# Optimization experiments

Measured on AMD Instinct MI355X. Metric: run time of the kernel, lower is better.

Reference implementation:

```python
import jax, jax.numpy as jnp
import numpy as np

EPS = 1e-6
NORM_FACTOR = 1000.0  # self.normalization_factor, aggregation 'sum'

# ---- Lorentz manifold (curvature -1, hyperboloid <x,x>_L = -1) ----

def _linner(x, y):
    # Lorentz inner product, keepdim on last axis
    return -x[..., :1] * y[..., :1] + jnp.sum(x[..., 1:] * y[..., 1:], axis=-1, keepdims=True)

def _proj_tan0(u):
    return jnp.concatenate([jnp.zeros_like(u[..., :1]), u[..., 1:]], axis=-1)

def _expmap0(u):
    sp = u[..., 1:]
    n = jnp.sqrt(jnp.clip(jnp.sum(sp * sp, axis=-1, keepdims=True), EPS))
    return jnp.concatenate([jnp.cosh(n), jnp.sinh(n) / n * sp], axis=-1)

def _logmap0(x):
    x0 = jnp.clip(x[..., :1], 1.0 + EPS)
    d = jnp.arccosh(x0)
    sp = x[..., 1:] * (d / jnp.sqrt(x0 * x0 - 1.0))
    return jnp.concatenate([jnp.zeros_like(x0), sp], axis=-1)

def _dist(x, y):
    return jnp.arccosh(jnp.clip(-_linner(x, y), 1.0 + EPS))

def _logmap(x, y):
    alpha = jnp.clip(-_linner(x, y), 1.0 + EPS)
    u = y - alpha * x                      # y + <x,y>_L x
    return jnp.arccosh(alpha) * u / jnp.sqrt(alpha * alpha - 1.0)

def _expmap(x, u):
    n = jnp.sqrt(jnp.clip(_linner(u, u), EPS))
    return jnp.cosh(n) * x + jnp.sinh(n) / n * u

def _proju(x, u):
    return u + _linner(x, u) * x

def _transp0(y, v):
    # parallel transport from origin o=(1,0,...,0) to y
    coef = _linner(y, v) / (1.0 + y[..., :1])
    oy = jnp.concatenate([y[..., :1] + 1.0, y[..., 1:]], axis=-1)
    return v + coef * oy

def _layernorm(x, g, b, eps=1e-5):
    m = jnp.mean(x, axis=-1, keepdims=True)
    v = jnp.mean((x - m) ** 2, axis=-1, keepdims=True)
    return (x - m) / jnp.sqrt(v + eps) * g + b


def setup_inputs() -> dict:
    N, E, D, ED = 10000, 320000, 128, 2
    key = jax.random.key(0)
    ks = jax.random.split(key, 10)
    # nodes on the hyperboloid: expmap0 of a small tangent vector
    h_tan = 0.02 * jax.random.normal(ks[0], (N, D), dtype=jnp.float32)
    h = _expmap0(_proj_tan0(h_tan))
    edge_attr = jax.random.normal(ks[1], (E, ED), dtype=jnp.float32)
    row = jax.random.randint(ks[2], (E,), 0, N, dtype=jnp.int32)
    col = jax.random.randint(ks[3], (E,), 0, N, dtype=jnp.int32)
    node_mask = jnp.ones((N, 1), dtype=jnp.float32)
    edge_mask = jnp.ones((E, 1), dtype=jnp.float32)
    s = 1.0 / np.sqrt(D)
    W = s * jax.random.normal(ks[4], (D, D), dtype=jnp.float32)
    bias = 0.0 * jax.random.normal(ks[5], (1, D), dtype=jnp.float32)  # init.constant_(bias, 0)
    att_in = 2 * D + ED + 1  # x_row, x_col, edge_attr + geodesic
    att_w1 = (1.0 / np.sqrt(att_in)) * jax.random.normal(ks[6], (att_in, D), dtype=jnp.float32)
    att_b1 = jnp.zeros((D,), dtype=jnp.float32)
    att_w2 = s * jax.random.normal(ks[7], (D, 1), dtype=jnp.float32)
    att_b2 = jnp.zeros((1,), dtype=jnp.float32)
    ln_gamma = jnp.ones((D - 1,), dtype=jnp.float32)
    ln_beta = jnp.zeros((D - 1,), dtype=jnp.float32)
    return {"h": h, "edge_attr": edge_attr, "row": row, "col": col,
            "node_mask": node_mask, "edge_mask": edge_mask, "W": W, "bias": bias,
            "att_w1": att_w1, "att_b1": att_b1, "att_w2": att_w2, "att_b2": att_b2,
            "ln_gamma": ln_gamma, "ln_beta": ln_beta}


def reference(h, edge_attr, row, col, node_mask, edge_mask, W, bias,
              att_w1, att_b1, att_w2, att_b2, ln_gamma, ln_beta):
    N = h.shape[0]
    # ---- HypLinear ----
    xt = _logmap0(h) @ W                  # Linear(in,out,bias=False)
    x = _expmap0(_proj_tan0(xt))
    b = _transp0(x, _proj_tan0(bias))
    x = _expmap(x, b)
    # ---- HypAgg ----
    x_tan = _logmap0(x)
    xr, xc = x[row], x[col]
    geo = _dist(xr, xc)                   # [E,1]
    att_in = jnp.concatenate([x_tan[row], x_tan[col], edge_attr, geo], axis=-1)
    hid = jax.nn.silu(att_in @ att_w1 + att_b1)
    att = jax.nn.sigmoid(hid @ att_w2 + att_b2) * edge_mask   # [E,1]
    loc = _logmap(xr, xc)                 # [E,D]
    agg = jax.ops.segment_sum(loc * att, row, num_segments=N) / NORM_FACTOR
    x = _expmap(x, _proju(x, agg))
    # ---- HNorm (Lorentz: LN on spatial components only) ----
    ht = _logmap0(x)
    sp = _layernorm(ht[..., 1:], ln_gamma, ln_beta)
    x = _expmap0(jnp.concatenate([ht[..., :1], sp], axis=-1))
    # ---- HypAct (manifold_out = Lorentz as well) ----
    xt = _proj_tan0(jax.nn.silu(_logmap0(x)))
    return _expmap0(xt)
```

## Files before the change

kernel.cpp:

```cpp
#include <hip/hip_runtime.h>
#include <math.h>

#define D 128
#define NPB 8
#define EPS1 (1.0f + 1e-6f)

__device__ __forceinline__ float sum16(float v) {
#pragma unroll
    for (int o = 8; o; o >>= 1) v += __shfl_xor(v, o, 64);
    return v;
}

__device__ __forceinline__ float facosh(float a) {
    return __logf(a + sqrtf(fmaxf(a * a - 1.0f, 0.0f)));
}

__device__ __forceinline__ void unpack8(const float4& a, const float4& b,
                                        float* d) {
    d[0] = a.x; d[1] = a.y; d[2] = a.z; d[3] = a.w;
    d[4] = b.x; d[5] = b.y; d[6] = b.z; d[7] = b.w;
}

__device__ __forceinline__ void bsumH(float* v, float (*wred)[4], int lane,
                                      int wid, int kp) {
    __syncthreads();
#pragma unroll
    for (int o = 32; o; o >>= 1)
#pragma unroll
        for (int nl = 0; nl < 4; nl++) v[nl] += __shfl_xor(v[nl], o, 64);
    if (lane == 0)
#pragma unroll
        for (int nl = 0; nl < 4; nl++) wred[wid][nl] = v[nl];
    __syncthreads();
#pragma unroll
    for (int nl = 0; nl < 4; nl++)
        v[nl] = wred[2 * kp][nl] + wred[2 * kp + 1][nl];
}

__global__ __launch_bounds__(256) void node_pre8(
    const float* __restrict__ h, const float* __restrict__ W,
    const float* __restrict__ bias, const float* __restrict__ att_w1,
    const float* __restrict__ att_b1, float* __restrict__ XQ,
    float* __restrict__ P_out, const int* __restrict__ row,
    int* __restrict__ cnt, int N, int E) {
    int i0 = blockIdx.x * NPB;
    int tid = threadIdx.x;
    int j = tid & 127, kp = tid >> 7;
    int lane = tid & 63, wid = tid >> 6;
    int nbase = kp * 4;
    __shared__ __align__(16) float t8[NPB][D];
    __shared__ float psumP[2][NPB][D];
    __shared__ float psumQ[2][NPB][D];
    __shared__ float wred[4][4];

    float hj[4];
#pragma unroll
    for (int nl = 0; nl < 4; nl++) {
        int gi = i0 + nbase + nl;
        hj[nl] = (gi < N) ? h[(size_t)gi * D + j] : 0.0f;
        t8[nbase + nl][j] = hj[nl];
    }
    __syncthreads();
    float tj[4];
#pragma unroll
    for (int nl = 0; nl < 4; nl++) {
        float h0 = fmaxf(t8[nbase + nl][0], EPS1);
        float fac = facosh(h0) * rsqrtf(h0 * h0 - 1.0f);
        tj[nl] = (j == 0) ? 0.0f : hj[nl] * fac;
    }
    __syncthreads();
#pragma unroll
    for (int nl = 0; nl < 4; nl++) t8[nbase + nl][j] = tj[nl];
    __syncthreads();

    float xtp[NPB];
#pragma unroll
    for (int n = 0; n < NPB; n++) xtp[n] = 0.0f;
    int kbeg = kp * 64;
    for (int k0 = kbeg; k0 < kbeg + 64; k0 += 4) {
        float w0 = W[(k0 + 0) * D + j], w1 = W[(k0 + 1) * D + j];
        float w2 = W[(k0 + 2) * D + j], w3 = W[(k0 + 3) * D + j];
#pragma unroll
        for (int n = 0; n < NPB; n++) {
            float4 tv = *(const float4*)&t8[n][k0];
            xtp[n] = fmaf(tv.x, w0,
                          fmaf(tv.y, w1, fmaf(tv.z, w2, fmaf(tv.w, w3, xtp[n]))));
        }
    }
#pragma unroll
    for (int n = 0; n < NPB; n++) psumP[kp][n][j] = xtp[n];
    __syncthreads();
    float xt[4];
#pragma unroll
    for (int nl = 0; nl < 4; nl++) {
        int n = nbase + nl;
        xt[nl] = (j == 0) ? 0.0f : (psumP[0][n][j] + psumP[1][n][j]);
    }

    float v4[4];
#pragma unroll
    for (int nl = 0; nl < 4; nl++) v4[nl] = xt[nl] * xt[nl];
    bsumH(v4, wred, lane, wid, kp);
    float xj[4];
#pragma unroll
    for (int nl = 0; nl < 4; nl++) {
        float nn = sqrtf(fmaxf(v4[nl], 1e-6f));
        float e = __expf(nn), ei = __fdividef(1.0f, e);
        float ch = 0.5f * (e + ei), sh = 0.5f * (e - ei);
        xj[nl] = (j == 0) ? ch : __fdividef(sh, nn) * xt[nl];
    }

    float vj = (j == 0) ? 0.0f : bias[j];
#pragma unroll
    for (int nl = 0; nl < 4; nl++) v4[nl] = xj[nl] * vj;
    bsumH(v4, wred, lane, wid, kp);
    __syncthreads();
#pragma unroll
    for (int nl = 0; nl < 4; nl++) t8[nbase + nl][j] = xj[nl];
    __syncthreads();
    float bj[4];
#pragma unroll
    for (int nl = 0; nl < 4; nl++) {
        float X0 = t8[nbase + nl][0];
        float coef = __fdividef(v4[nl], 1.0f + X0);
        bj[nl] = vj + coef * ((j == 0) ? (X0 + 1.0f) : xj[nl]);
    }
#pragma unroll
    for (int nl = 0; nl < 4; nl++)
        v4[nl] = (j == 0) ? -bj[nl] * bj[nl] : bj[nl] * bj[nl];
    bsumH(v4, wred, lane, wid, kp);
    float xnj[4];
#pragma unroll
    for (int nl = 0; nl < 4; nl++) {
        float nb = sqrtf(fmaxf(v4[nl], 1e-6f));
        float e = __expf(nb), ei = __fdividef(1.0f, e);
        float ch = 0.5f * (e + ei), sh = 0.5f * (e - ei);
        xnj[nl] = ch * xj[nl] + __fdividef(sh, nb) * bj[nl];
        int gi = i0 + nbase + nl;
        if (gi < N) XQ[(size_t)gi * 256 + j] = xnj[nl];
    }

    __syncthreads();
#pragma unroll
    for (int nl = 0; nl < 4; nl++) t8[nbase + nl][j] = xnj[nl];
    __syncthreads();
    float xtj[4];
#pragma unroll
    for (int nl = 0; nl < 4; nl++) {
        float Y0 = fmaxf(t8[nbase + nl][0], EPS1);
        float f = facosh(Y0) * rsqrtf(Y0 * Y0 - 1.0f);
        xtj[nl] = (j == 0) ? 0.0f : xnj[nl] * f;
    }
    __syncthreads();
#pragma unroll
    for (int nl = 0; nl < 4; nl++) t8[nbase + nl][j] = xtj[nl];
    __syncthreads();

    float pp[NPB], qq[NPB];
#pragma unroll
    for (int n = 0; n < NPB; n++) {
        pp[n] = 0.0f;
        qq[n] = 0.0f;
    }
    for (int k0 = kbeg; k0 < kbeg + 64; k0 += 4) {
        float a0 = att_w1[(k0 + 0) * D + j], a1 = att_w1[(k0 + 1) * D + j];
        float a2 = att_w1[(k0 + 2) * D + j], a3 = att_w1[(k0 + 3) * D + j];
        float c0 = att_w1[(D + k0 + 0) * D + j], c1 = att_w1[(D + k0 + 1) * D + j];
        float c2 = att_w1[(D + k0 + 2) * D + j], c3 = att_w1[(D + k0 + 3) * D + j];
#pragma unroll
        for (int n = 0; n < NPB; n++) {
            float4 tv = *(const float4*)&t8[n][k0];
            pp[n] = fmaf(tv.x, a0,
                         fmaf(tv.y, a1, fmaf(tv.z, a2, fmaf(tv.w, a3, pp[n]))));
            qq[n] = fmaf(tv.x, c0,
                         fmaf(tv.y, c1, fmaf(tv.z, c2, fmaf(tv.w, c3, qq[n]))));
        }
    }
#pragma unroll
    for (int n = 0; n < NPB; n++) {
        psumP[kp][n][j] = pp[n];
        psumQ[kp][n][j] = qq[n];
    }
    __syncthreads();
    float b1 = att_b1[j];
#pragma unroll
    for (int nl = 0; nl < 4; nl++) {
        int n = nbase + nl;
        int gi = i0 + n;
        if (gi < N) {
            P_out[(size_t)gi * D + j] = psumP[0][n][j] + psumP[1][n][j] + b1;
            XQ[(size_t)gi * 256 + 128 + j] = psumQ[0][n][j] + psumQ[1][n][j];
        }
    }

    int gtid = blockIdx.x * 256 + tid;
    int tot = gridDim.x * 256;
    for (int e2 = gtid; e2 < E; e2 += tot) atomicAdd(&cnt[row[e2]], 1);
}

__global__ __launch_bounds__(1024) void scan_kernel(const int* __restrict__ cnt,
                                                    int* __restrict__ off,
                                                    int* __restrict__ cursor,
                                                    int N) {
    __shared__ int wsum[16];
    __shared__ int carry_s;
    int tid = threadIdx.x, lane = tid & 63, wid = tid >> 6;
    if (tid == 0) carry_s = 0;
    __syncthreads();
    for (int base = 0; base < N; base += 1024) {
        int idx = base + tid;
        int v = (idx < N) ? cnt[idx] : 0;
        int orig = v;
#pragma unroll
        for (int o = 1; o < 64; o <<= 1) {
            int t = __shfl_up(v, o, 64);
            if (lane >= o) v += t;
        }
        if (lane == 63) wsum[wid] = v;
        __syncthreads();
        if (wid == 0 && lane < 16) {
            int w = wsum[lane];
#pragma unroll
            for (int o = 1; o < 16; o <<= 1) {
                int t = __shfl_up(w, o, 64);
                if (lane >= o) w += t;
            }
            wsum[lane] = w;
        }
        __syncthreads();
        int carry = carry_s;
        int wbase = (wid == 0) ? 0 : wsum[wid - 1];
        int excl = carry + wbase + v - orig;
        if (idx < N) {
            off[idx] = excl;
            cursor[idx] = excl;
        }
        __syncthreads();
        if (tid == 1023) carry_s = carry + wsum[15];
        __syncthreads();
    }
}

__global__ void scatter_kernel(const int* __restrict__ row,
                               const int* __restrict__ col,
                               const float* __restrict__ edge_attr,
                               const float* __restrict__ edge_mask,
                               int* __restrict__ cursor,
                               float4* __restrict__ rec, int E) {
    const float2* ea2 = (const float2*)edge_attr;
    for (int e = blockIdx.x * blockDim.x + threadIdx.x; e < E;
         e += gridDim.x * blockDim.x) {
        int r = row[e];
        int pos = atomicAdd(&cursor[r], 1);
        float2 a = ea2[e];
        rec[pos] = make_float4(__int_as_float(col[e]), a.x, a.y, edge_mask[e]);
    }
}

__global__ __launch_bounds__(256) void edge_agg(
    const float* __restrict__ XQ, const float* __restrict__ P,
    const float4* __restrict__ rec, const int* __restrict__ off,
    const int* __restrict__ cnt, const float* __restrict__ w1c,
    const float* __restrict__ att_w2, const float* __restrict__ att_b2,
    float* __restrict__ agg, int N) {
    int tid = threadIdx.x, lane = tid & 63;
    int sub = lane & 15, grp = lane >> 4;
    int i = blockIdx.x * 4 + (tid >> 6);
    bool valid = i < N;
    i = min(i, N - 1);
    int f4 = sub * 2;

    const float4* w4 = (const float4*)w1c;
    const float4* aw4 = (const float4*)att_w2;
    const float4* xq4r = (const float4*)(XQ + (size_t)i * 256);
    const float4* pr4 = (const float4*)(P + (size_t)i * D);
    float xr[8], pr[8], wa[8], wb[8], wg[8], w2v[8];
    unpack8(xq4r[f4], xq4r[f4 + 1], xr);
    unpack8(pr4[f4], pr4[f4 + 1], pr);
    unpack8(w4[f4], w4[f4 + 1], wa);
    unpack8(w4[32 + f4], w4[32 + f4 + 1], wb);
    unpack8(w4[64 + f4], w4[64 + f4 + 1], wg);
    unpack8(aw4[f4], aw4[f4 + 1], w2v);
    float b2 = att_b2[0];
    float xr0s = (sub == 0) ? -xr[0] : xr[0];

    float acc[8];
#pragma unroll
    for (int u = 0; u < 8; u++) acc[u] = 0.0f;

    int s = off[i], m = valid ? cnt[i] : 0;
    int clen = (m + 3) >> 2;
    int k0 = grp * clen;
    int len = min(m, k0 + clen) - k0;

    auto compute2 = [&](const float4& rc1, const float4& a0, const float4& a1,
                        const float4& a2, const float4& a3, bool act1,
                        const float4& rc2, const float4& b0, const float4& b1,
                        const float4& b2q, const float4& b3, bool act2) {
        float xc1[8], qc1[8], xc2[8], qc2[8];
        unpack8(a0, a1, xc1);
        unpack8(a2, a3, qc1);
        unpack8(b0, b1, xc2);
        unpack8(b2q, b3, qc2);
        float lin1 = xr0s * xc1[0];
        float lin2 = xr0s * xc2[0];
#pragma unroll
        for (int u = 1; u < 8; u++) {
            lin1 = fmaf(xr[u], xc1[u], lin1);
            lin2 = fmaf(xr[u], xc2[u], lin2);
        }
#pragma unroll
        for (int o = 8; o; o >>= 1) {
            lin1 += __shfl_xor(lin1, o, 64);
            lin2 += __shfl_xor(lin2, o, 64);
        }
        float alpha1 = fmaxf(-lin1, EPS1);
        float alpha2 = fmaxf(-lin2, EPS1);
        float a2m1 = fmaxf(fmaf(alpha1, alpha1, -1.0f), 1e-12f);
        float a2m2 = fmaxf(fmaf(alpha2, alpha2, -1.0f), 1e-12f);
        float rden1 = rsqrtf(a2m1);
        float rden2 = rsqrtf(a2m2);
        float geo1 = __logf(fmaf(a2m1, rden1, alpha1));
        float geo2 = __logf(fmaf(a2m2, rden2, alpha2));
        float lp1 = 0.0f, lp2 = 0.0f;
#pragma unroll
        for (int u = 0; u < 8; u++) {
            float hv1 = pr[u] + qc1[u] +
                        fmaf(rc1.y, wa[u], fmaf(rc1.z, wb[u], geo1 * wg[u]));
            float hv2 = pr[u] + qc2[u] +
                        fmaf(rc2.y, wa[u], fmaf(rc2.z, wb[u], geo2 * wg[u]));
            float sg1 = __fdividef(1.0f, 1.0f + __expf(-hv1));
            float sg2 = __fdividef(1.0f, 1.0f + __expf(-hv2));
            lp1 = fmaf(hv1 * sg1, w2v[u], lp1);
            lp2 = fmaf(hv2 * sg2, w2v[u], lp2);
        }
#pragma unroll
        for (int o = 8; o; o >>= 1) {
            lp1 += __shfl_xor(lp1, o, 64);
            lp2 += __shfl_xor(lp2, o, 64);
        }
        float w1 = act1 ? rc1.w : 0.0f;
        float w2 = act2 ? rc2.w : 0.0f;
        float att1 = w1 * __fdividef(1.0f, 1.0f + __expf(-(lp1 + b2)));
        float att2 = w2 * __fdividef(1.0f, 1.0f + __expf(-(lp2 + b2)));
        float sc1 = att1 * geo1 * rden1 * 1e-3f;
        float sc2 = att2 * geo2 * rden2 * 1e-3f;
#pragma unroll
        for (int u = 0; u < 8; u++) {
            acc[u] = fmaf(sc1, fmaf(-alpha1, xr[u], xc1[u]), acc[u]);
            acc[u] = fmaf(sc2, fmaf(-alpha2, xr[u], xc2[u]), acc[u]);
        }
    };

    float4 z = make_float4(__int_as_float(0), 0.0f, 0.0f, 0.0f);
    float4 rcA = z, rcB = z, rcC, rcD;
    if (len > 0) rcA = rec[s + k0];
    if (len > 1) rcB = rec[s + k0 + 1];
    const float4* pA = (const float4*)(XQ + (size_t)__float_as_int(rcA.x) * 256);
    const float4* pB = (const float4*)(XQ + (size_t)__float_as_int(rcB.x) * 256);
    float4 gA0 = pA[f4], gA1 = pA[f4 + 1], gA2 = pA[32 + f4],
           gA3 = pA[32 + f4 + 1];
    float4 gB0 = pB[f4], gB1 = pB[f4 + 1], gB2 = pB[32 + f4],
           gB3 = pB[32 + f4 + 1];

    for (int t = 0; t < clen; t += 2) {
        rcC = rcA;
        if (t + 2 < len) rcC = rec[s + k0 + t + 2];
        rcD = rcB;
        if (t + 3 < len) rcD = rec[s + k0 + t + 3];
        const float4* pC =
            (const float4*)(XQ + (size_t)__float_as_int(rcC.x) * 256);
        const float4* pD =
            (const float4*)(XQ + (size_t)__float_as_int(rcD.x) * 256);
        float4 gC0 = pC[f4], gC1 = pC[f4 + 1], gC2 = pC[32 + f4],
               gC3 = pC[32 + f4 + 1];
        float4 gD0 = pD[f4], gD1 = pD[f4 + 1], gD2 = pD[32 + f4],
               gD3 = pD[32 + f4 + 1];
        compute2(rcA, gA0, gA1, gA2, gA3, t < len, rcB, gB0, gB1, gB2, gB3,
                 t + 1 < len);
        rcA = rcC; rcB = rcD;
        gA0 = gC0; gA1 = gC1; gA2 = gC2; gA3 = gC3;
        gB0 = gD0; gB1 = gD1; gB2 = gD2; gB3 = gD3;
    }

#pragma unroll
    for (int u = 0; u < 8; u++) {
        acc[u] += __shfl_xor(acc[u], 16, 64);
        acc[u] += __shfl_xor(acc[u], 32, 64);
    }
    if (valid && grp == 0) {
        float4* a4 = (float4*)(agg + (size_t)i * D);
        a4[f4] = make_float4(acc[0], acc[1], acc[2], acc[3]);
        a4[f4 + 1] = make_float4(acc[4], acc[5], acc[6], acc[7]);
    }
}

__global__ __launch_bounds__(256) void node_post(
    const float* __restrict__ XQ, const float* __restrict__ agg,
    const float* __restrict__ gamma, const float* __restrict__ beta,
    float* __restrict__ out, int N) {
    int tid = threadIdx.x, lane = tid & 63;
    int sub = lane & 15;
    int i = blockIdx.x * 16 + (tid >> 4);
    bool valid = i < N;
    i = min(i, N - 1);
    int j8 = sub * 8, f4 = sub * 2;

    const float4* xq4r = (const float4*)(XQ + (size_t)i * 256);
    const float4* ag4 = (const float4*)(agg + (size_t)i * D);
    float xr[8], acc[8];
    unpack8(xq4r[f4], xq4r[f4 + 1], xr);
    unpack8(ag4[f4], ag4[f4 + 1], acc);

    float lxa_p = (sub == 0) ? -xr[0] * acc[0] : xr[0] * acc[0];
#pragma unroll
    for (int u = 1; u < 8; u++) lxa_p = fmaf(xr[u], acc[u], lxa_p);
    float lxa = sum16(lxa_p);
    float uj[8];
#pragma unroll
    for (int u = 0; u < 8; u++) uj[u] = fmaf(lxa, xr[u], acc[u]);
    float luu_p = (sub == 0) ? -uj[0] * uj[0] : uj[0] * uj[0];
#pragma unroll
    for (int u = 1; u < 8; u++) luu_p = fmaf(uj[u], uj[u], luu_p);
    float luu = sum16(luu_p);
    float nn = sqrtf(fmaxf(luu, 1e-6f));
    float e = __expf(nn), ei = __fdividef(1.0f, e);
    float ch = 0.5f * (e + ei), shv = __fdividef(0.5f * (e - ei), nn);
    float xn[8];
#pragma unroll
    for (int u = 0; u < 8; u++) xn[u] = ch * xr[u] + shv * uj[u];
    float X0 = __shfl(xn[0], lane & 48, 64);
    X0 = fmaxf(X0, EPS1);
    float fc = facosh(X0) * rsqrtf(X0 * X0 - 1.0f);
    float ht[8];
#pragma unroll
    for (int u = 0; u < 8; u++) ht[u] = xn[u] * fc;
    if (sub == 0) ht[0] = 0.0f;
    float mp = 0.0f;
#pragma unroll
    for (int u = 0; u < 8; u++) mp += ht[u];
    float mean = sum16(mp) * (1.0f / 127.0f);
    float diff[8];
#pragma unroll
    for (int u = 0; u < 8; u++) diff[u] = ht[u] - mean;
    if (sub == 0) diff[0] = 0.0f;
    float vp = 0.0f;
#pragma unroll
    for (int u = 0; u < 8; u++) vp = fmaf(diff[u], diff[u], vp);
    float var = sum16(vp) * (1.0f / 127.0f);
    float rstd = rsqrtf(var + 1e-5f);
    float sp[8];
#pragma unroll
    for (int u = 0; u < 8; u++) {
        int j = j8 + u;
        sp[u] = (j > 0) ? fmaf(diff[u] * rstd, gamma[j - 1], beta[j - 1]) : 0.0f;
    }
    float n2p = 0.0f;
#pragma unroll
    for (int u = 0; u < 8; u++) n2p = fmaf(sp[u], sp[u], n2p);
    float n2 = sqrtf(fmaxf(sum16(n2p), 1e-6f));
    e = __expf(n2);
    ei = __fdividef(1.0f, e);
    float y0 = 0.5f * (e + ei), sh2 = __fdividef(0.5f * (e - ei), n2);
    float yj[8];
#pragma unroll
    for (int u = 0; u < 8; u++) yj[u] = sh2 * sp[u];
    if (sub == 0) yj[0] = y0;
    float y0c = fmaxf(y0, EPS1);
    float f3 = facosh(y0c) * rsqrtf(y0c * y0c - 1.0f);
    float sj[8];
#pragma unroll
    for (int u = 0; u < 8; u++) {
        float lj = yj[u] * f3;
        sj[u] = __fdividef(lj, 1.0f + __expf(-lj));
    }
    if (sub == 0) sj[0] = 0.0f;
    float n3p = 0.0f;
#pragma unroll
    for (int u = 0; u < 8; u++) n3p = fmaf(sj[u], sj[u], n3p);
    float n3 = sqrtf(fmaxf(sum16(n3p), 1e-6f));
    e = __expf(n3);
    ei = __fdividef(1.0f, e);
    float o0 = 0.5f * (e + ei), sh3 = __fdividef(0.5f * (e - ei), n3);
    float ov[8];
#pragma unroll
    for (int u = 0; u < 8; u++) ov[u] = sh3 * sj[u];
    if (sub == 0) ov[0] = o0;
    if (valid) {
        float4* o4 = (float4*)(out + (size_t)i * D);
        o4[f4] = make_float4(ov[0], ov[1], ov[2], ov[3]);
        o4[f4 + 1] = make_float4(ov[4], ov[5], ov[6], ov[7]);
    }
}

extern "C" void kernel_launch(void* const* d_in, const int* in_sizes, int n_in,
                              void* d_out, int out_size, void* d_ws,
                              size_t ws_size, hipStream_t stream) {
    const float* h = (const float*)d_in[0];
    const float* edge_attr = (const float*)d_in[1];
    const int* row = (const int*)d_in[2];
    const int* col = (const int*)d_in[3];
    const float* edge_mask = (const float*)d_in[5];
    const float* W = (const float*)d_in[6];
    const float* bias = (const float*)d_in[7];
    const float* att_w1 = (const float*)d_in[8];
    const float* att_b1 = (const float*)d_in[9];
    const float* att_w2 = (const float*)d_in[10];
    const float* att_b2 = (const float*)d_in[11];
    const float* ln_g = (const float*)d_in[12];
    const float* ln_b = (const float*)d_in[13];

    int N = in_sizes[0] / D;
    int E = in_sizes[2];

    float* XQ = (float*)d_ws;
    float* Pbuf = XQ + (size_t)N * 256;
    float4* rec = (float4*)(Pbuf + (size_t)N * D);
    int* cnt = (int*)(rec + E);
    int* off = cnt + N;
    int* cur = off + N;
    float* aggb = (float*)(cur + N);

    hipMemsetAsync(cnt, 0, N * sizeof(int), stream);
    node_pre8<<<(N + NPB - 1) / NPB, 256, 0, stream>>>(
        h, W, bias, att_w1, att_b1, XQ, Pbuf, row, cnt, N, E);
    scan_kernel<<<1, 1024, 0, stream>>>(cnt, off, cur, N);
    scatter_kernel<<<640, 256, 0, stream>>>(row, col, edge_attr, edge_mask,
                                            cur, rec, E);
    edge_agg<<<(N + 3) / 4, 256, 0, stream>>>(XQ, Pbuf, rec, off, cnt,
                                              att_w1 + 256 * D, att_w2, att_b2,
                                              aggb, N);
    node_post<<<(N + 15) / 16, 256, 0, stream>>>(XQ, aggb, ln_g, ln_b,
                                                 (float*)d_out, N);
}
```

Baseline: 153.7 us.

## Fuse node_post into edge_agg, use DPP row reductions, simplify edge pipeline

Merges the node post-processing (expmap, layernorm, activation) into the tail of the edge aggregation kernel. This removes the agg buffer round trip and one kernel launch. The 16-lane shuffle reductions become DPP row_shr reductions, which are cheaper than ds_swizzle/bpermute shuffles. The two-edge interleaved compute loop is replaced by a single-edge compute with a simpler one-ahead prefetch, lowering register pressure at the cost of less instruction-level parallelism. Post work now runs redundantly in all four lane groups, and only group 0 writes.

```diff
diff --git a/kernel.cpp b/kernel.cpp
--- a/kernel.cpp
+++ b/kernel.cpp
@@ -5,9 +5,15 @@
 #define NPB 8
 #define EPS1 (1.0f + 1e-6f)
 
-__device__ __forceinline__ float sum16(float v) {
-#pragma unroll
-    for (int o = 8; o; o >>= 1) v += __shfl_xor(v, o, 64);
+__device__ __forceinline__ float dpp_rsum16(float v) {
+    v += __int_as_float(__builtin_amdgcn_update_dpp(
+        0, __float_as_int(v), 0x121, 0xf, 0xf, true));
+    v += __int_as_float(__builtin_amdgcn_update_dpp(
+        0, __float_as_int(v), 0x122, 0xf, 0xf, true));
+    v += __int_as_float(__builtin_amdgcn_update_dpp(
+        0, __float_as_int(v), 0x124, 0xf, 0xf, true));
+    v += __int_as_float(__builtin_amdgcn_update_dpp(
+        0, __float_as_int(v), 0x128, 0xf, 0xf, true));
     return v;
 }
 
@@ -262,13 +268,14 @@
     const float4* __restrict__ rec, const int* __restrict__ off,
     const int* __restrict__ cnt, const float* __restrict__ w1c,
     const float* __restrict__ att_w2, const float* __restrict__ att_b2,
-    float* __restrict__ agg, int N) {
+    const float* __restrict__ gamma, const float* __restrict__ beta,
+    float* __restrict__ out, int N) {
     int tid = threadIdx.x, lane = tid & 63;
     int sub = lane & 15, grp = lane >> 4;
     int i = blockIdx.x * 4 + (tid >> 6);
     bool valid = i < N;
     i = min(i, N - 1);
-    int f4 = sub * 2;
+    int j8 = sub * 8, f4 = sub * 2;
 
     const float4* w4 = (const float4*)w1c;
     const float4* aw4 = (const float4*)att_w2;
@@ -293,94 +300,57 @@
     int k0 = grp * clen;
     int len = min(m, k0 + clen) - k0;
 
-    auto compute2 = [&](const float4& rc1, const float4& a0, const float4& a1,
-                        const float4& a2, const float4& a3, bool act1,
-                        const float4& rc2, const float4& b0, const float4& b1,
-                        const float4& b2q, const float4& b3, bool act2) {
-        float xc1[8], qc1[8], xc2[8], qc2[8];
-        unpack8(a0, a1, xc1);
-        unpack8(a2, a3, qc1);
-        unpack8(b0, b1, xc2);
-        unpack8(b2q, b3, qc2);
-        float lin1 = xr0s * xc1[0];
-        float lin2 = xr0s * xc2[0];
-#pragma unroll
-        for (int u = 1; u < 8; u++) {
-            lin1 = fmaf(xr[u], xc1[u], lin1);
-            lin2 = fmaf(xr[u], xc2[u], lin2);
-        }
-#pragma unroll
-        for (int o = 8; o; o >>= 1) {
-            lin1 += __shfl_xor(lin1, o, 64);
-            lin2 += __shfl_xor(lin2, o, 64);
-        }
-        float alpha1 = fmaxf(-lin1, EPS1);
-        float alpha2 = fmaxf(-lin2, EPS1);
-        float a2m1 = fmaxf(fmaf(alpha1, alpha1, -1.0f), 1e-12f);
-        float a2m2 = fmaxf(fmaf(alpha2, alpha2, -1.0f), 1e-12f);
-        float rden1 = rsqrtf(a2m1);
-        float rden2 = rsqrtf(a2m2);
-        float geo1 = __logf(fmaf(a2m1, rden1, alpha1));
-        float geo2 = __logf(fmaf(a2m2, rden2, alpha2));
-        float lp1 = 0.0f, lp2 = 0.0f;
+    auto compute = [&](const float4& rc, const float4& g0, const float4& g1,
+                       const float4& g2, const float4& g3, bool act) {
+        float xc[8], qc[8];
+        unpack8(g0, g1, xc);
+        unpack8(g2, g3, qc);
+        float lin = xr0s * xc[0];
+#pragma unroll
+        for (int u = 1; u < 8; u++) lin = fmaf(xr[u], xc[u], lin);
+        lin = dpp_rsum16(lin);
+        float alpha = fmaxf(-lin, EPS1);
+        float a2m = fmaxf(fmaf(alpha, alpha, -1.0f), 1e-12f);
+        float rden = rsqrtf(a2m);
+        float geo = __logf(fmaf(a2m, rden, alpha));
+        float lp = 0.0f;
 #pragma unroll
         for (int u = 0; u < 8; u++) {
-            float hv1 = pr[u] + qc1[u] +
-                        fmaf(rc1.y, wa[u], fmaf(rc1.z, wb[u], geo1 * wg[u]));
-            float hv2 = pr[u] + qc2[u] +
-                        fmaf(rc2.y, wa[u], fmaf(rc2.z, wb[u], geo2 * wg[u]));
-            float sg1 = __fdividef(1.0f, 1.0f + __expf(-hv1));
-            float sg2 = __fdividef(1.0f, 1.0f + __expf(-hv2));
-            lp1 = fmaf(hv1 * sg1, w2v[u], lp1);
-            lp2 = fmaf(hv2 * sg2, w2v[u], lp2);
-        }
-#pragma unroll
-        for (int o = 8; o; o >>= 1) {
-            lp1 += __shfl_xor(lp1, o, 64);
-            lp2 += __shfl_xor(lp2, o, 64);
-        }
-        float w1 = act1 ? rc1.w : 0.0f;
-        float w2 = act2 ? rc2.w : 0.0f;
-        float att1 = w1 * __fdividef(1.0f, 1.0f + __expf(-(lp1 + b2)));
-        float att2 = w2 * __fdividef(1.0f, 1.0f + __expf(-(lp2 + b2)));
-        float sc1 = att1 * geo1 * rden1 * 1e-3f;
-        float sc2 = att2 * geo2 * rden2 * 1e-3f;
-#pragma unroll
-        for (int u = 0; u < 8; u++) {
-            acc[u] = fmaf(sc1, fmaf(-alpha1, xr[u], xc1[u]), acc[u]);
-            acc[u] = fmaf(sc2, fmaf(-alpha2, xr[u], xc2[u]), acc[u]);
-        }
+            float hv = pr[u] + qc[u] +
+                       fmaf(rc.y, wa[u], fmaf(rc.z, wb[u], geo * wg[u]));
+            float sig = __fdividef(1.0f, 1.0f + __expf(-hv));
+            lp = fmaf(hv * sig, w2v[u], lp);
+        }
+        lp = dpp_rsum16(lp);
+        float w = act ? rc.w : 0.0f;
+        float att = w * __fdividef(1.0f, 1.0f + __expf(-(lp + b2)));
+        float scale = att * geo * rden * 1e-3f;
+#pragma unroll
+        for (int u = 0; u < 8; u++)
+            acc[u] = fmaf(scale, fmaf(-alpha, xr[u], xc[u]), acc[u]);
     };
 
-    float4 z = make_float4(__int_as_float(0), 0.0f, 0.0f, 0.0f);
-    float4 rcA = z, rcB = z, rcC, rcD;
+    float4 rcA = make_float4(__int_as_float(0), 0.0f, 0.0f, 0.0f), rcB;
     if (len > 0) rcA = rec[s + k0];
-    if (len > 1) rcB = rec[s + k0 + 1];
-    const float4* pA = (const float4*)(XQ + (size_t)__float_as_int(rcA.x) * 256);
-    const float4* pB = (const float4*)(XQ + (size_t)__float_as_int(rcB.x) * 256);
+    const float4* pA =
+        (const float4*)(XQ + (size_t)__float_as_int(rcA.x) * 256);
     float4 gA0 = pA[f4], gA1 = pA[f4 + 1], gA2 = pA[32 + f4],
            gA3 = pA[32 + f4 + 1];
-    float4 gB0 = pB[f4], gB1 = pB[f4 + 1], gB2 = pB[32 + f4],
-           gB3 = pB[32 + f4 + 1];
+    float4 gB0, gB1, gB2, gB3;
 
     for (int t = 0; t < clen; t += 2) {
-        rcC = rcA;
-        if (t + 2 < len) rcC = rec[s + k0 + t + 2];
-        rcD = rcB;
-        if (t + 3 < len) rcD = rec[s + k0 + t + 3];
-        const float4* pC =
-            (const float4*)(XQ + (size_t)__float_as_int(rcC.x) * 256);
-        const float4* pD =
-            (const float4*)(XQ + (size_t)__float_as_int(rcD.x) * 256);
-        float4 gC0 = pC[f4], gC1 = pC[f4 + 1], gC2 = pC[32 + f4],
-               gC3 = pC[32 + f4 + 1];
-        float4 gD0 = pD[f4], gD1 = pD[f4 + 1], gD2 = pD[32 + f4],
-               gD3 = pD[32 + f4 + 1];
-        compute2(rcA, gA0, gA1, gA2, gA3, t < len, rcB, gB0, gB1, gB2, gB3,
-                 t + 1 < len);
-        rcA = rcC; rcB = rcD;
-        gA0 = gC0; gA1 = gC1; gA2 = gC2; gA3 = gC3;
-        gB0 = gD0; gB1 = gD1; gB2 = gD2; gB3 = gD3;
+        rcB = rcA;
+        if (t + 1 < len) rcB = rec[s + k0 + t + 1];
+        const float4* pB =
+            (const float4*)(XQ + (size_t)__float_as_int(rcB.x) * 256);
+        gB0 = pB[f4]; gB1 = pB[f4 + 1]; gB2 = pB[32 + f4]; gB3 = pB[32 + f4 + 1];
+        compute(rcA, gA0, gA1, gA2, gA3, t < len);
+        rcA = rcB;
+        if (t + 2 < len) rcA = rec[s + k0 + t + 2];
+        const float4* pN =
+            (const float4*)(XQ + (size_t)__float_as_int(rcA.x) * 256);
+        gA0 = pN[f4]; gA1 = pN[f4 + 1]; gA2 = pN[32 + f4]; gA3 = pN[32 + f4 + 1];
+        compute(rcB, gB0, gB1, gB2, gB3, t + 1 < len);
     }
 
 #pragma unroll
@@ -388,41 +358,18 @@
         acc[u] += __shfl_xor(acc[u], 16, 64);
         acc[u] += __shfl_xor(acc[u], 32, 64);
     }
-    if (valid && grp == 0) {
-        float4* a4 = (float4*)(agg + (size_t)i * D);
-        a4[f4] = make_float4(acc[0], acc[1], acc[2], acc[3]);
-        a4[f4 + 1] = make_float4(acc[4], acc[5], acc[6], acc[7]);
-    }
-}
-
-__global__ __launch_bounds__(256) void node_post(
-    const float* __restrict__ XQ, const float* __restrict__ agg,
-    const float* __restrict__ gamma, const float* __restrict__ beta,
-    float* __restrict__ out, int N) {
-    int tid = threadIdx.x, lane = tid & 63;
-    int sub = lane & 15;
-    int i = blockIdx.x * 16 + (tid >> 4);
-    bool valid = i < N;
-    i = min(i, N - 1);
-    int j8 = sub * 8, f4 = sub * 2;
-
-    const float4* xq4r = (const float4*)(XQ + (size_t)i * 256);
-    const float4* ag4 = (const float4*)(agg + (size_t)i * D);
-    float xr[8], acc[8];
-    unpack8(xq4r[f4], xq4r[f4 + 1], xr);
-    unpack8(ag4[f4], ag4[f4 + 1], acc);
 
     float lxa_p = (sub == 0) ? -xr[0] * acc[0] : xr[0] * acc[0];
 #pragma unroll
     for (int u = 1; u < 8; u++) lxa_p = fmaf(xr[u], acc[u], lxa_p);
-    float lxa = sum16(lxa_p);
+    float lxa = dpp_rsum16(lxa_p);
     float uj[8];
 #pragma unroll
     for (int u = 0; u < 8; u++) uj[u] = fmaf(lxa, xr[u], acc[u]);
     float luu_p = (sub == 0) ? -uj[0] * uj[0] : uj[0] * uj[0];
 #pragma unroll
     for (int u = 1; u < 8; u++) luu_p = fmaf(uj[u], uj[u], luu_p);
-    float luu = sum16(luu_p);
+    float luu = dpp_rsum16(luu_p);
     float nn = sqrtf(fmaxf(luu, 1e-6f));
     float e = __expf(nn), ei = __fdividef(1.0f, e);
     float ch = 0.5f * (e + ei), shv = __fdividef(0.5f * (e - ei), nn);
@@ -439,7 +386,7 @@
     float mp = 0.0f;
 #pragma unroll
     for (int u = 0; u < 8; u++) mp += ht[u];
-    float mean = sum16(mp) * (1.0f / 127.0f);
+    float mean = dpp_rsum16(mp) * (1.0f / 127.0f);
     float diff[8];
 #pragma unroll
     for (int u = 0; u < 8; u++) diff[u] = ht[u] - mean;
@@ -447,7 +394,7 @@
     float vp = 0.0f;
 #pragma unroll
     for (int u = 0; u < 8; u++) vp = fmaf(diff[u], diff[u], vp);
-    float var = sum16(vp) * (1.0f / 127.0f);
+    float var = dpp_rsum16(vp) * (1.0f / 127.0f);
     float rstd = rsqrtf(var + 1e-5f);
     float sp[8];
 #pragma unroll
@@ -458,7 +405,7 @@
     float n2p = 0.0f;
 #pragma unroll
     for (int u = 0; u < 8; u++) n2p = fmaf(sp[u], sp[u], n2p);
-    float n2 = sqrtf(fmaxf(sum16(n2p), 1e-6f));
+    float n2 = sqrtf(fmaxf(dpp_rsum16(n2p), 1e-6f));
     e = __expf(n2);
     ei = __fdividef(1.0f, e);
     float y0 = 0.5f * (e + ei), sh2 = __fdividef(0.5f * (e - ei), n2);
@@ -478,7 +425,7 @@
     float n3p = 0.0f;
 #pragma unroll
     for (int u = 0; u < 8; u++) n3p = fmaf(sj[u], sj[u], n3p);
-    float n3 = sqrtf(fmaxf(sum16(n3p), 1e-6f));
+    float n3 = sqrtf(fmaxf(dpp_rsum16(n3p), 1e-6f));
     e = __expf(n3);
     ei = __fdividef(1.0f, e);
     float o0 = 0.5f * (e + ei), sh3 = __fdividef(0.5f * (e - ei), n3);
@@ -486,7 +433,7 @@
 #pragma unroll
     for (int u = 0; u < 8; u++) ov[u] = sh3 * sj[u];
     if (sub == 0) ov[0] = o0;
-    if (valid) {
+    if (valid && grp == 0) {
         float4* o4 = (float4*)(out + (size_t)i * D);
         o4[f4] = make_float4(ov[0], ov[1], ov[2], ov[3]);
         o4[f4 + 1] = make_float4(ov[4], ov[5], ov[6], ov[7]);
@@ -519,7 +466,6 @@
     int* cnt = (int*)(rec + E);
     int* off = cnt + N;
     int* cur = off + N;
-    float* aggb = (float*)(cur + N);
 
     hipMemsetAsync(cnt, 0, N * sizeof(int), stream);
     node_pre8<<<(N + NPB - 1) / NPB, 256, 0, stream>>>(
@@ -529,7 +475,5 @@
                                             cur, rec, E);
     edge_agg<<<(N + 3) / 4, 256, 0, stream>>>(XQ, Pbuf, rec, off, cnt,
                                               att_w1 + 256 * D, att_w2, att_b2,
-                                              aggb, N);
-    node_post<<<(N + 15) / 16, 256, 0, stream>>>(XQ, aggb, ln_g, ln_b,
-                                                 (float*)d_out, N);
-}
+                                              ln_g, ln_b, (float*)d_out, N);
+}
```

Result: faster. 146.4 us (-4.7%).
